# Kernel optimization log

Hardware: AMD Instinct MI355X
Metric: run time of the kernel (lower is better)

The kernel has to match this reference:

```python
import jax, jax.numpy as jnp
import numpy as np

B, L, H, V = 16, 512, 256, 32000
HALF = H // 2
EPS_LN = 1e-5
EPS_NORM = 1e-12


def setup_inputs() -> dict:
    key = jax.random.key(0)
    ks = jax.random.split(key, 9)
    s = 0.02
    return {
        "seq": jax.random.randint(ks[0], (B, L), 0, V),
        "embed": jax.random.normal(ks[1], (V, H), jnp.float32) * s,
        "W1": jax.random.normal(ks[2], (2 * H, H), jnp.float32) * s,
        "b1": jnp.zeros((2 * H,), jnp.float32),
        "W2": jax.random.normal(ks[3], (H, 2 * H), jnp.float32) * s,
        "b2": jnp.zeros((H,), jnp.float32),
        "gamma": jnp.ones((H,), jnp.float32),
        "beta": jnp.zeros((H,), jnp.float32),
        "W_sem": jax.random.normal(ks[4], (HALF, H), jnp.float32) * s,
        "W_epi": jax.random.normal(ks[5], (HALF, H), jnp.float32) * s,
        "W_rp": jax.random.normal(ks[6], (H, H), jnp.float32) * s,
        "b_rp": jnp.zeros((H,), jnp.float32),
        "W_out": jax.random.normal(ks[7], (V, H), jnp.float32) * s,
        "b_out": jnp.zeros((V,), jnp.float32),
    }


def _l2norm(x):
    # F.normalize(dim=-1): x / max(||x||, eps)
    n = jnp.sqrt(jnp.sum(x * x, axis=-1, keepdims=True))
    return x / jnp.maximum(n, EPS_NORM)


def reference(seq, embed, W1, b1, W2, b2, gamma, beta, W_sem, W_epi, W_rp, b_rp, W_out, b_out):
    h = embed[seq]                                   # [B, L, H]
    ff = jnp.maximum(h @ W1.T + b1, 0.0) @ W2.T + b2  # MLP with 2H hidden
    x = h + ff
    mu = jnp.mean(x, axis=-1, keepdims=True)
    var = jnp.var(x, axis=-1, keepdims=True)
    h = (x - mu) / jnp.sqrt(var + EPS_LN) * gamma + beta  # LayerNorm

    ks_all = jnp.einsum('blh,kh->blk', h, W_sem)     # [B, L, HALF]
    ke_all = jnp.einsum('blh,kh->blk', h, W_epi)

    def step(carry, kv):
        M_s, M_e = carry
        k_s, k_e = kv                                 # [B, HALF] each
        kns = _l2norm(k_s)
        kne = _l2norm(k_e)
        vps = jnp.einsum('bij,bj->bi', M_s, kns)      # read from fast weights
        vpe = jnp.einsum('bij,bj->bi', M_e, kne)
        M_s = M_s + jnp.einsum('bi,bj->bij', k_s - vps, kns)  # delta-rule write
        M_e = M_e + jnp.einsum('bi,bj->bij', k_e - vpe, kne)
        return (M_s, M_e), None

    M0 = jnp.zeros((B, HALF, HALF), h.dtype)
    # scan over timesteps 0..L-2 (time-major)
    (M_s, M_e), _ = jax.lax.scan(
        step, (M0, M0),
        (jnp.swapaxes(ks_all[:, :-1], 0, 1), jnp.swapaxes(ke_all[:, :-1], 0, 1)))

    cs = jnp.einsum('bij,bj->bi', M_s, ks_all[:, -1])  # read with last-token query
    ce = jnp.einsum('bij,bj->bi', M_e, ke_all[:, -1])
    c = jnp.concatenate([cs, ce], axis=-1)             # [B, H]
    r = c @ W_rp.T + b_rp
    return r @ W_out.T + b_out                          # [B, V]
```

## Files before the change

kernel.cpp:

```cpp
#include <hip/hip_runtime.h>

#define B_ 16
#define L_ 512
#define H_ 256
#define V_ 32000
#define HALF_ 128

typedef __attribute__((ext_vector_type(8))) short short8;
typedef __attribute__((ext_vector_type(4))) float floatx4;

__device__ __forceinline__ unsigned short f2bf(float x) {
  unsigned int u = __float_as_uint(x);
  unsigned int r = (u + 0x7FFFu + ((u >> 16) & 1u)) >> 16;
  return (unsigned short)r;
}

template <int CTRL>
__device__ __forceinline__ float dpp_xor_add(float x) {
  int y = __builtin_amdgcn_mov_dpp(__float_as_int(x), CTRL, 0xf, 0xf, true);
  return x + __int_as_float(y);
}

__device__ __forceinline__ float redu16(float p) {
  p = dpp_xor_add<0xB1>(p);
  p = dpp_xor_add<0x4E>(p);
  p = dpp_xor_add<0x141>(p);
  p = dpp_xor_add<0x140>(p);
  return p;
}

__device__ __forceinline__ void async_cp16(const float* g, float* l) {
  __builtin_amdgcn_global_load_lds(
      (const __attribute__((address_space(1))) void*)g,
      (__attribute__((address_space(3))) void*)l, 16, 0, 0);
}

__device__ __forceinline__ uint4 load8cvt(const float* p) {
  float4 a = ((const float4*)p)[0];
  float4 b = ((const float4*)p)[1];
  uint4 r;
  r.x = (unsigned)f2bf(a.x) | ((unsigned)f2bf(a.y) << 16);
  r.y = (unsigned)f2bf(a.z) | ((unsigned)f2bf(a.w) << 16);
  r.z = (unsigned)f2bf(b.x) | ((unsigned)f2bf(b.y) << 16);
  r.w = (unsigned)f2bf(b.z) | ((unsigned)f2bf(b.w) << 16);
  return r;
}

__global__ __launch_bounds__(256) void gemm1_kernel(const int* __restrict__ seq,
                                                    const float* __restrict__ embed,
                                                    const float* __restrict__ W1,
                                                    const float* __restrict__ b1,
                                                    unsigned short* __restrict__ a1b) {
  __shared__ unsigned short As[128 * 40];
  __shared__ unsigned short Bs[128 * 40];
  int tid = threadIdx.x;
  int wave = tid >> 6, lane = tid & 63;
  int wm = (wave >> 1) * 64, wn = (wave & 1) * 64;
  int quad = lane >> 4, l15 = lane & 15;
  int bm = blockIdx.y * 128, bn = blockIdx.x * 128;
  int sr = tid >> 2, sq = tid & 3;

  int tok0 = seq[bm + sr];
  int tok1 = seq[bm + 64 + sr];

  floatx4 zero = {0.f, 0.f, 0.f, 0.f};
  floatx4 acc[4][4];
#pragma unroll
  for (int fi = 0; fi < 4; fi++)
#pragma unroll
    for (int fj = 0; fj < 4; fj++) acc[fi][fj] = zero;

  uint4 av0 = load8cvt(embed + (size_t)tok0 * H_ + sq * 8);
  uint4 av1 = load8cvt(embed + (size_t)tok1 * H_ + sq * 8);
  uint4 bv0 = load8cvt(W1 + (size_t)(bn + sr) * 256 + sq * 8);
  uint4 bv1 = load8cvt(W1 + (size_t)(bn + 64 + sr) * 256 + sq * 8);

  for (int k0 = 0; k0 < 256; k0 += 32) {
    __syncthreads();
    *(uint4*)(As + sr * 40 + sq * 8) = av0;
    *(uint4*)(As + (64 + sr) * 40 + sq * 8) = av1;
    *(uint4*)(Bs + sr * 40 + sq * 8) = bv0;
    *(uint4*)(Bs + (64 + sr) * 40 + sq * 8) = bv1;
    __syncthreads();
    if (k0 + 32 < 256) {
      av0 = load8cvt(embed + (size_t)tok0 * H_ + k0 + 32 + sq * 8);
      av1 = load8cvt(embed + (size_t)tok1 * H_ + k0 + 32 + sq * 8);
      bv0 = load8cvt(W1 + (size_t)(bn + sr) * 256 + k0 + 32 + sq * 8);
      bv1 = load8cvt(W1 + (size_t)(bn + 64 + sr) * 256 + k0 + 32 + sq * 8);
    }
    short8 af[4], bf[4];
#pragma unroll
    for (int f = 0; f < 4; f++) {
      af[f] = *(const short8*)(As + (wm + f * 16 + l15) * 40 + quad * 8);
      bf[f] = *(const short8*)(Bs + (wn + f * 16 + l15) * 40 + quad * 8);
    }
#pragma unroll
    for (int fi = 0; fi < 4; fi++)
#pragma unroll
      for (int fj = 0; fj < 4; fj++)
        acc[fi][fj] = __builtin_amdgcn_mfma_f32_16x16x32_bf16(af[fi], bf[fj], acc[fi][fj], 0, 0, 0);
  }

#pragma unroll
  for (int fi = 0; fi < 4; fi++) {
#pragma unroll
    for (int fj = 0; fj < 4; fj++) {
      int col = bn + wn + fj * 16 + l15;
      float bb = b1[col];
#pragma unroll
      for (int rg = 0; rg < 4; rg++) {
        int row = bm + wm + fi * 16 + quad * 4 + rg;
        float v = fmaxf(acc[fi][fj][rg] + bb, 0.f);
        a1b[(size_t)row * 512 + col] = f2bf(v);
      }
    }
  }
}

__global__ __launch_bounds__(256) void mlp2_kernel(const unsigned short* __restrict__ a1b,
                                                   const float* __restrict__ W2,
                                                   const float* __restrict__ b2,
                                                   const int* __restrict__ seq,
                                                   const float* __restrict__ embed,
                                                   const float* __restrict__ gamma,
                                                   const float* __restrict__ beta,
                                                   unsigned short* __restrict__ hnb) {
  __shared__ unsigned short As[32 * 40];
  __shared__ unsigned short Bs[256 * 40];
  __shared__ float stats[2][2][32];
  int tid = threadIdx.x;
  int wave = tid >> 6, lane = tid & 63;
  int wm = (wave >> 1) * 16, wnh = wave & 1, wn = wnh * 128;
  int quad = lane >> 4, l15 = lane & 15;
  int bm = blockIdx.x * 32;
  int sr = tid >> 2, sq = tid & 3;

  floatx4 zero = {0.f, 0.f, 0.f, 0.f};
  floatx4 acc[8];
#pragma unroll
  for (int fj = 0; fj < 8; fj++) acc[fj] = zero;

  uint4 av, bv[4];
  if (tid < 128) av = *(const uint4*)(a1b + (size_t)(bm + sr) * 512 + sq * 8);
#pragma unroll
  for (int q = 0; q < 4; q++) {
    int unit = q * 256 + tid;
    bv[q] = load8cvt(W2 + (size_t)(unit >> 2) * 512 + (unit & 3) * 8);
  }

  for (int k0 = 0; k0 < 512; k0 += 32) {
    __syncthreads();
    if (tid < 128) *(uint4*)(As + sr * 40 + sq * 8) = av;
#pragma unroll
    for (int q = 0; q < 4; q++) {
      int unit = q * 256 + tid;
      *(uint4*)(Bs + (unit >> 2) * 40 + (unit & 3) * 8) = bv[q];
    }
    __syncthreads();
    if (k0 + 32 < 512) {
      if (tid < 128) av = *(const uint4*)(a1b + (size_t)(bm + sr) * 512 + k0 + 32 + sq * 8);
#pragma unroll
      for (int q = 0; q < 4; q++) {
        int unit = q * 256 + tid;
        bv[q] = load8cvt(W2 + (size_t)(unit >> 2) * 512 + k0 + 32 + (unit & 3) * 8);
      }
    }
    short8 af = *(const short8*)(As + (wm + l15) * 40 + quad * 8);
    short8 bf[8];
#pragma unroll
    for (int fj = 0; fj < 8; fj++)
      bf[fj] = *(const short8*)(Bs + (wn + fj * 16 + l15) * 40 + quad * 8);
#pragma unroll
    for (int fj = 0; fj < 8; fj++)
      acc[fj] = __builtin_amdgcn_mfma_f32_16x16x32_bf16(af, bf[fj], acc[fj], 0, 0, 0);
  }

  int seqv[4];
#pragma unroll
  for (int rg = 0; rg < 4; rg++) seqv[rg] = seq[bm + wm + quad * 4 + rg];
  float v[8][4];
#pragma unroll
  for (int fj = 0; fj < 8; fj++) {
    int col = wn + fj * 16 + l15;
    float bb = b2[col];
#pragma unroll
    for (int rg = 0; rg < 4; rg++)
      v[fj][rg] = acc[fj][rg] + bb + embed[(size_t)seqv[rg] * H_ + col];
  }
  float s_[4], q_[4];
#pragma unroll
  for (int rg = 0; rg < 4; rg++) {
    float s = 0.f, q = 0.f;
#pragma unroll
    for (int fj = 0; fj < 8; fj++) {
      s += v[fj][rg];
      q += v[fj][rg] * v[fj][rg];
    }
    s_[rg] = redu16(s);
    q_[rg] = redu16(q);
  }
  if (l15 == 0) {
#pragma unroll
    for (int rg = 0; rg < 4; rg++) {
      int rlocal = wm + quad * 4 + rg;
      stats[wnh][0][rlocal] = s_[rg];
      stats[wnh][1][rlocal] = q_[rg];
    }
  }
  __syncthreads();
  float mu[4], inv[4];
#pragma unroll
  for (int rg = 0; rg < 4; rg++) {
    int rlocal = wm + quad * 4 + rg;
    float sum = stats[0][0][rlocal] + stats[1][0][rlocal];
    float ssq = stats[0][1][rlocal] + stats[1][1][rlocal];
    mu[rg] = sum * (1.f / H_);
    float var = ssq * (1.f / H_) - mu[rg] * mu[rg];
    inv[rg] = rsqrtf(var + 1e-5f);
  }
#pragma unroll
  for (int fj = 0; fj < 8; fj++) {
    int col = wn + fj * 16 + l15;
    float g = gamma[col], be = beta[col];
#pragma unroll
    for (int rg = 0; rg < 4; rg++) {
      int row = bm + wm + quad * 4 + rg;
      float y = (v[fj][rg] - mu[rg]) * inv[rg] * g + be;
      hnb[(size_t)row * H_ + col] = f2bf(y);
    }
  }
}

__global__ __launch_bounds__(256) void kproj_kernel(const unsigned short* __restrict__ hnb,
                                                    const float* __restrict__ Ws,
                                                    const float* __restrict__ We,
                                                    float* __restrict__ khat,
                                                    float* __restrict__ kT) {
  __shared__ unsigned short As[32 * 40];
  __shared__ unsigned short Bs[256 * 40];
  int tid = threadIdx.x;
  int wave = tid >> 6, lane = tid & 63;
  int wm = (wave >> 1) * 16, wnh = wave & 1, wn = wnh * 128;
  int quad = lane >> 4, l15 = lane & 15;
  int bm = blockIdx.x * 32;
  int sr = tid >> 2, sq = tid & 3;

  floatx4 zero = {0.f, 0.f, 0.f, 0.f};
  floatx4 acc[8];
#pragma unroll
  for (int fj = 0; fj < 8; fj++) acc[fj] = zero;

  uint4 av, bv[4];
  if (tid < 128) av = *(const uint4*)(hnb + (size_t)(bm + sr) * H_ + sq * 8);
#pragma unroll
  for (int q = 0; q < 4; q++) {
    int unit = q * 256 + tid;
    int row = unit >> 2;
    const float* src = (row < 128) ? (Ws + (size_t)row * H_) : (We + (size_t)(row - 128) * H_);
    bv[q] = load8cvt(src + (unit & 3) * 8);
  }

  for (int k0 = 0; k0 < 256; k0 += 32) {
    __syncthreads();
    if (tid < 128) *(uint4*)(As + sr * 40 + sq * 8) = av;
#pragma unroll
    for (int q = 0; q < 4; q++) {
      int unit = q * 256 + tid;
      *(uint4*)(Bs + (unit >> 2) * 40 + (unit & 3) * 8) = bv[q];
    }
    __syncthreads();
    if (k0 + 32 < 256) {
      if (tid < 128) av = *(const uint4*)(hnb + (size_t)(bm + sr) * H_ + k0 + 32 + sq * 8);
#pragma unroll
      for (int q = 0; q < 4; q++) {
        int unit = q * 256 + tid;
        int row = unit >> 2;
        const float* src = (row < 128) ? (Ws + (size_t)row * H_) : (We + (size_t)(row - 128) * H_);
        bv[q] = load8cvt(src + k0 + 32 + (unit & 3) * 8);
      }
    }
    short8 af = *(const short8*)(As + (wm + l15) * 40 + quad * 8);
    short8 bf[8];
#pragma unroll
    for (int fj = 0; fj < 8; fj++)
      bf[fj] = *(const short8*)(Bs + (wn + fj * 16 + l15) * 40 + quad * 8);
#pragma unroll
    for (int fj = 0; fj < 8; fj++)
      acc[fj] = __builtin_amdgcn_mfma_f32_16x16x32_bf16(af, bf[fj], acc[fj], 0, 0, 0);
  }

  int b = bm >> 9;
  int idxm = b * 2 + wnh;
  int tloc0 = (bm & 511) + wm + quad * 4;
  float inv[4];
#pragma unroll
  for (int rg = 0; rg < 4; rg++) {
    float ssq = 0.f;
#pragma unroll
    for (int fj = 0; fj < 8; fj++) ssq += acc[fj][rg] * acc[fj][rg];
    ssq = redu16(ssq);
    inv[rg] = 1.f / fmaxf(sqrtf(ssq), 1e-12f);
  }
#pragma unroll
  for (int fj = 0; fj < 8; fj++) {
    int ch = fj * 16 + l15;
    int j = ch >> 2, e = ch & 3;
    int pj = (j & 1) ? (16 + (j >> 1)) : (j >> 1);
    int pcol = pj * 4 + e;
#pragma unroll
    for (int rg = 0; rg < 4; rg++)
      khat[((size_t)idxm * L_ + tloc0 + rg) * HALF_ + pcol] = acc[fj][rg] * inv[rg];
    float4 raw = {acc[fj][0], acc[fj][1], acc[fj][2], acc[fj][3]};
    *(float4*)(kT + (size_t)idxm * (HALF_ * L_) + (size_t)ch * L_ + tloc0) = raw;
  }
}

#define STEP(KP, KR)                                                     \
  do {                                                                   \
    float t0_ = m[0] * KP[0] + m[1] * KP[1];                             \
    float t1_ = m[2] * KP[2] + m[3] * KP[3];                             \
    float t2_ = m[4] * KP[4] + m[5] * KP[5];                             \
    float t3_ = m[6] * KP[6] + m[7] * KP[7];                             \
    float p_ = (t0_ + t1_) + (t2_ + t3_);                                \
    p_ = redu16(p_);                                                     \
    float s_ = (KR) - p_;                                                \
    m[0] += s_ * KP[0]; m[1] += s_ * KP[1]; m[2] += s_ * KP[2];          \
    m[3] += s_ * KP[3]; m[4] += s_ * KP[4]; m[5] += s_ * KP[5];          \
    m[6] += s_ * KP[6]; m[7] += s_ * KP[7];                              \
  } while (0)

__global__ __launch_bounds__(512) void scan_kernel(const float* __restrict__ khat,
                                                   const float* __restrict__ kT,
                                                   float* __restrict__ c) {
  __shared__ float sk[2][64 * 128];
  int bid = blockIdx.x;
  int idxm = bid & 31;
  int rgp = bid >> 5;
  int b = idxm >> 1, mat = idxm & 1;
  const float* kh = khat + (size_t)idxm * L_ * HALF_;
  const float* kTi = kT + (size_t)idxm * HALF_ * L_;

  int tid = threadIdx.x;
  int wave = tid >> 6, lane = tid & 63;
  int seg = tid & 15, rl = tid >> 4;
  int r = rgp * 32 + rl;
  int c0 = seg * 8;
  const float* krow = kTi + (size_t)r * L_;

  float m[8];
#pragma unroll
  for (int g = 0; g < 8; g++) m[g] = 0.f;

  {
#pragma unroll
    for (int j = 0; j < 4; j++) {
      int slice = j * 8 + wave;
      async_cp16(kh + slice * 256 + lane * 4, &sk[0][slice * 256] + lane * 4);
    }
  }
  __syncthreads();

  float4 krn = *(const float4*)(krow);
  const float* lb = &sk[0][0] + seg * 4;

  for (int ch = 0; ch < 7; ch++) {
    {
#pragma unroll
      for (int j = 0; j < 4; j++) {
        int slice = j * 8 + wave;
        async_cp16(kh + (size_t)(ch + 1) * 8192 + slice * 256 + lane * 4,
                   &sk[(ch + 1) & 1][slice * 256] + lane * 4);
      }
    }
    const float* base = lb + (ch & 1) * 8192;
    float pk[4][8];
#pragma unroll
    for (int u = 0; u < 4; u++) {
      *(float4*)&pk[u][0] = *(const float4*)(base + u * 128);
      *(float4*)&pk[u][4] = *(const float4*)(base + u * 128 + 64);
    }
    for (int g = 0; g < 15; g++) {
      float4 krc = krn;
      krn = *(const float4*)(krow + ch * 64 + g * 4 + 4);
#pragma unroll
      for (int u = 0; u < 4; u++) {
        STEP(pk[u], ((u == 0) ? krc.x : (u == 1) ? krc.y : (u == 2) ? krc.z : krc.w));
        int tn = g * 4 + u + 4;
        *(float4*)&pk[u][0] = *(const float4*)(base + tn * 128);
        *(float4*)&pk[u][4] = *(const float4*)(base + tn * 128 + 64);
      }
    }
    {
      float4 krc = krn;
      krn = *(const float4*)(krow + ch * 64 + 64);
      STEP(pk[0], krc.x);
      STEP(pk[1], krc.y);
      STEP(pk[2], krc.z);
      STEP(pk[3], krc.w);
    }
    __syncthreads();
  }

  {
    const float* base = lb + 8192;
    float pk[4][8];
#pragma unroll
    for (int u = 0; u < 4; u++) {
      *(float4*)&pk[u][0] = *(const float4*)(base + u * 128);
      *(float4*)&pk[u][4] = *(const float4*)(base + u * 128 + 64);
    }
    for (int g = 0; g < 15; g++) {
      float4 krc = krn;
      krn = *(const float4*)(krow + 448 + g * 4 + 4);
#pragma unroll
      for (int u = 0; u < 4; u++) {
        STEP(pk[u], ((u == 0) ? krc.x : (u == 1) ? krc.y : (u == 2) ? krc.z : krc.w));
        int tn = g * 4 + u + 4;
        *(float4*)&pk[u][0] = *(const float4*)(base + tn * 128);
        *(float4*)&pk[u][4] = *(const float4*)(base + tn * 128 + 64);
      }
    }
    float4 krc = krn;
    STEP(pk[0], krc.x);
    STEP(pk[1], krc.y);
    STEP(pk[2], krc.z);
  }

  float q[8];
#pragma unroll
  for (int j = 0; j < 8; j++) q[j] = kTi[(size_t)(c0 + j) * L_ + 511];
  float t0 = m[0] * q[0] + m[1] * q[1];
  float t1 = m[2] * q[2] + m[3] * q[3];
  float t2 = m[4] * q[4] + m[5] * q[5];
  float t3 = m[6] * q[6] + m[7] * q[7];
  float p = redu16((t0 + t1) + (t2 + t3));
  if (seg == 0) c[(size_t)b * H_ + mat * HALF_ + r] = p;
}

__global__ void rp_kernel(const float* __restrict__ c, const float* __restrict__ Wrp,
                          const float* __restrict__ brp, float* __restrict__ r) {
  int b = blockIdx.x;
  int n = threadIdx.x;
  __shared__ float cs[H_];
  cs[n] = c[(size_t)b * H_ + n];
  __syncthreads();
  const float4* w4 = (const float4*)(Wrp + (size_t)n * H_);
  const float4* c4 = (const float4*)cs;
  float acc = 0.f;
#pragma unroll 8
  for (int k = 0; k < H_ / 4; k++) {
    float4 w = w4[k], cc = c4[k];
    acc += w.x * cc.x + w.y * cc.y + w.z * cc.z + w.w * cc.w;
  }
  r[(size_t)b * H_ + n] = acc + brp[n];
}

__global__ __launch_bounds__(256) void out_kernel(const float* __restrict__ r,
                                                  const float* __restrict__ Wout,
                                                  const float* __restrict__ bout,
                                                  float* __restrict__ out) {
  __shared__ float rs[16 * 272];
  __shared__ float obuf[16 * 68];
  int tid = threadIdx.x;
#pragma unroll
  for (int q = 0; q < 16; q++) {
    int idx = q * 256 + tid;
    int bb = idx >> 8, cc = idx & 255;
    rs[bb * 272 + cc + 4 * (cc >> 6)] = r[idx];
  }
  __syncthreads();
  int row = tid >> 2, part = tid & 3;
  int v = blockIdx.x * 64 + row;
  const float4* w4 = (const float4*)(Wout + (size_t)v * H_ + part * 64);
  float acc[16];
#pragma unroll
  for (int bb = 0; bb < 16; bb++) acc[bb] = 0.f;
#pragma unroll 4
  for (int j = 0; j < 16; j++) {
    float4 w = w4[j];
#pragma unroll
    for (int bb = 0; bb < 16; bb++) {
      float4 rv = *(const float4*)&rs[bb * 272 + part * 68 + j * 4];
      acc[bb] += w.x * rv.x + w.y * rv.y + w.z * rv.z + w.w * rv.w;
    }
  }
  float bo = bout[v];
#pragma unroll
  for (int bb = 0; bb < 16; bb++) {
    acc[bb] = dpp_xor_add<0xB1>(acc[bb]);
    acc[bb] = dpp_xor_add<0x4E>(acc[bb]);
  }
#pragma unroll
  for (int q = 0; q < 4; q++) {
    int bb = part * 4 + q;
    obuf[bb * 68 + row] = acc[bb] + bo;
  }
  __syncthreads();
#pragma unroll
  for (int q = 0; q < 4; q++) {
    int idx = q * 256 + tid;
    int bb = idx >> 6, vl = idx & 63;
    out[(size_t)bb * V_ + blockIdx.x * 64 + vl] = obuf[bb * 68 + vl];
  }
}

extern "C" void kernel_launch(void* const* d_in, const int* in_sizes, int n_in,
                              void* d_out, int out_size, void* d_ws, size_t ws_size,
                              hipStream_t stream) {
  const int* seq = (const int*)d_in[0];
  const float* embed = (const float*)d_in[1];
  const float* W1 = (const float*)d_in[2];
  const float* b1 = (const float*)d_in[3];
  const float* W2 = (const float*)d_in[4];
  const float* b2 = (const float*)d_in[5];
  const float* gamma = (const float*)d_in[6];
  const float* beta = (const float*)d_in[7];
  const float* Wsem = (const float*)d_in[8];
  const float* Wepi = (const float*)d_in[9];
  const float* Wrp = (const float*)d_in[10];
  const float* brp = (const float*)d_in[11];
  const float* Wout = (const float*)d_in[12];
  const float* bout = (const float*)d_in[13];
  float* out = (float*)d_out;

  float* ws = (float*)d_ws;
  unsigned short* a1b = (unsigned short*)ws;
  unsigned short* hnb = (unsigned short*)(ws + 2097152);
  float* khat = ws + 3145728;
  float* kT = ws + 5242880;
  float* c = ws + 7340032;
  float* r = ws + 7344128;

  gemm1_kernel<<<dim3(4, 64), 256, 0, stream>>>(seq, embed, W1, b1, a1b);
  mlp2_kernel<<<256, 256, 0, stream>>>(a1b, W2, b2, seq, embed, gamma, beta, hnb);
  kproj_kernel<<<256, 256, 0, stream>>>(hnb, Wsem, Wepi, khat, kT);
  scan_kernel<<<128, 512, 0, stream>>>(khat, kT, c);
  rp_kernel<<<16, 256, 0, stream>>>(c, Wrp, brp, r);
  out_kernel<<<500, 256, 0, stream>>>(r, Wout, bout, out);
}
```

Before: 243.9 us.

## Chunk delta-rule scan with Gram-matrix triangular solve, fuse kproj into MLP

The sequential delta-rule scan is replaced by a chunked form. For each 16-token chunk, an MFMA computes the Gram matrix of the normalized keys, the corrections are found by forward substitution using readlane broadcasts, and the fast-weight updates are applied in a batch. This removes the per-step dependent read-update chain. The key-projection GEMM is fused into the MLP/LayerNorm kernel through an LDS-resident normalized tile, and a prep kernel pre-converts the weights to bf16 once per call. The scan grid also changes to 256 blocks of 256 threads. The Gram matrix is computed in bf16, which adds rounding error to the recurrence.

```diff
diff --git a/kernel.cpp b/kernel.cpp
--- a/kernel.cpp
+++ b/kernel.cpp
@@ -46,9 +46,23 @@
   return r;
 }
 
+__global__ __launch_bounds__(256) void prep_kernel(const float* __restrict__ W1,
+                                                   const float* __restrict__ W2,
+                                                   const float* __restrict__ Ws,
+                                                   const float* __restrict__ We,
+                                                   unsigned short* __restrict__ W1b,
+                                                   unsigned short* __restrict__ W2b,
+                                                   unsigned short* __restrict__ Wcb) {
+  int i = blockIdx.x * 256 + threadIdx.x;
+  if (i < 131072) W1b[i] = f2bf(W1[i]);
+  else if (i < 262144) W2b[i - 131072] = f2bf(W2[i - 131072]);
+  else if (i < 294912) Wcb[i - 262144] = f2bf(Ws[i - 262144]);
+  else Wcb[i - 262144] = f2bf(We[i - 294912]);
+}
+
 __global__ __launch_bounds__(256) void gemm1_kernel(const int* __restrict__ seq,
                                                     const float* __restrict__ embed,
-                                                    const float* __restrict__ W1,
+                                                    const unsigned short* __restrict__ W1b,
                                                     const float* __restrict__ b1,
                                                     unsigned short* __restrict__ a1b) {
   __shared__ unsigned short As[128 * 40];
@@ -72,8 +86,8 @@
 
   uint4 av0 = load8cvt(embed + (size_t)tok0 * H_ + sq * 8);
   uint4 av1 = load8cvt(embed + (size_t)tok1 * H_ + sq * 8);
-  uint4 bv0 = load8cvt(W1 + (size_t)(bn + sr) * 256 + sq * 8);
-  uint4 bv1 = load8cvt(W1 + (size_t)(bn + 64 + sr) * 256 + sq * 8);
+  uint4 bv0 = *(const uint4*)(W1b + (size_t)(bn + sr) * 256 + sq * 8);
+  uint4 bv1 = *(const uint4*)(W1b + (size_t)(bn + 64 + sr) * 256 + sq * 8);
 
   for (int k0 = 0; k0 < 256; k0 += 32) {
     __syncthreads();
@@ -85,8 +99,8 @@
     if (k0 + 32 < 256) {
       av0 = load8cvt(embed + (size_t)tok0 * H_ + k0 + 32 + sq * 8);
       av1 = load8cvt(embed + (size_t)tok1 * H_ + k0 + 32 + sq * 8);
-      bv0 = load8cvt(W1 + (size_t)(bn + sr) * 256 + k0 + 32 + sq * 8);
-      bv1 = load8cvt(W1 + (size_t)(bn + 64 + sr) * 256 + k0 + 32 + sq * 8);
+      bv0 = *(const uint4*)(W1b + (size_t)(bn + sr) * 256 + k0 + 32 + sq * 8);
+      bv1 = *(const uint4*)(W1b + (size_t)(bn + 64 + sr) * 256 + k0 + 32 + sq * 8);
     }
     short8 af[4], bf[4];
 #pragma unroll
@@ -117,16 +131,19 @@
   }
 }
 
-__global__ __launch_bounds__(256) void mlp2_kernel(const unsigned short* __restrict__ a1b,
-                                                   const float* __restrict__ W2,
+__global__ __launch_bounds__(256) void mlpk_kernel(const unsigned short* __restrict__ a1b,
+                                                   const unsigned short* __restrict__ W2b,
                                                    const float* __restrict__ b2,
                                                    const int* __restrict__ seq,
                                                    const float* __restrict__ embed,
                                                    const float* __restrict__ gamma,
                                                    const float* __restrict__ beta,
-                                                   unsigned short* __restrict__ hnb) {
+                                                   const unsigned short* __restrict__ Wcb,
+                                                   float* __restrict__ khat,
+                                                   float* __restrict__ kT) {
   __shared__ unsigned short As[32 * 40];
   __shared__ unsigned short Bs[256 * 40];
+  __shared__ unsigned short hnS[32 * 264];
   __shared__ float stats[2][2][32];
   int tid = threadIdx.x;
   int wave = tid >> 6, lane = tid & 63;
@@ -145,9 +162,8 @@
 #pragma unroll
   for (int q = 0; q < 4; q++) {
     int unit = q * 256 + tid;
-    bv[q] = load8cvt(W2 + (size_t)(unit >> 2) * 512 + (unit & 3) * 8);
-  }
-
+    bv[q] = *(const uint4*)(W2b + (size_t)(unit >> 2) * 512 + (unit & 3) * 8);
+  }
   for (int k0 = 0; k0 < 512; k0 += 32) {
     __syncthreads();
     if (tid < 128) *(uint4*)(As + sr * 40 + sq * 8) = av;
@@ -162,7 +178,7 @@
 #pragma unroll
       for (int q = 0; q < 4; q++) {
         int unit = q * 256 + tid;
-        bv[q] = load8cvt(W2 + (size_t)(unit >> 2) * 512 + k0 + 32 + (unit & 3) * 8);
+        bv[q] = *(const uint4*)(W2b + (size_t)(unit >> 2) * 512 + k0 + 32 + (unit & 3) * 8);
       }
     }
     short8 af = *(const short8*)(As + (wm + l15) * 40 + quad * 8);
@@ -208,61 +224,33 @@
     }
   }
   __syncthreads();
-  float mu[4], inv[4];
 #pragma unroll
   for (int rg = 0; rg < 4; rg++) {
     int rlocal = wm + quad * 4 + rg;
     float sum = stats[0][0][rlocal] + stats[1][0][rlocal];
     float ssq = stats[0][1][rlocal] + stats[1][1][rlocal];
-    mu[rg] = sum * (1.f / H_);
-    float var = ssq * (1.f / H_) - mu[rg] * mu[rg];
-    inv[rg] = rsqrtf(var + 1e-5f);
-  }
-#pragma unroll
-  for (int fj = 0; fj < 8; fj++) {
-    int col = wn + fj * 16 + l15;
-    float g = gamma[col], be = beta[col];
-#pragma unroll
-    for (int rg = 0; rg < 4; rg++) {
-      int row = bm + wm + quad * 4 + rg;
-      float y = (v[fj][rg] - mu[rg]) * inv[rg] * g + be;
-      hnb[(size_t)row * H_ + col] = f2bf(y);
-    }
-  }
-}
-
-__global__ __launch_bounds__(256) void kproj_kernel(const unsigned short* __restrict__ hnb,
-                                                    const float* __restrict__ Ws,
-                                                    const float* __restrict__ We,
-                                                    float* __restrict__ khat,
-                                                    float* __restrict__ kT) {
-  __shared__ unsigned short As[32 * 40];
-  __shared__ unsigned short Bs[256 * 40];
-  int tid = threadIdx.x;
-  int wave = tid >> 6, lane = tid & 63;
-  int wm = (wave >> 1) * 16, wnh = wave & 1, wn = wnh * 128;
-  int quad = lane >> 4, l15 = lane & 15;
-  int bm = blockIdx.x * 32;
-  int sr = tid >> 2, sq = tid & 3;
-
-  floatx4 zero = {0.f, 0.f, 0.f, 0.f};
-  floatx4 acc[8];
-#pragma unroll
-  for (int fj = 0; fj < 8; fj++) acc[fj] = zero;
-
-  uint4 av, bv[4];
-  if (tid < 128) av = *(const uint4*)(hnb + (size_t)(bm + sr) * H_ + sq * 8);
+    float mu = sum * (1.f / H_);
+    float var = ssq * (1.f / H_) - mu * mu;
+    float inv = rsqrtf(var + 1e-5f);
+#pragma unroll
+    for (int fj = 0; fj < 8; fj++) {
+      int col = wn + fj * 16 + l15;
+      float y = (v[fj][rg] - mu) * inv * gamma[col] + beta[col];
+      hnS[rlocal * 264 + col] = f2bf(y);
+    }
+  }
+  __syncthreads();
+
+  floatx4 acc2[8];
+#pragma unroll
+  for (int fj = 0; fj < 8; fj++) acc2[fj] = zero;
 #pragma unroll
   for (int q = 0; q < 4; q++) {
     int unit = q * 256 + tid;
-    int row = unit >> 2;
-    const float* src = (row < 128) ? (Ws + (size_t)row * H_) : (We + (size_t)(row - 128) * H_);
-    bv[q] = load8cvt(src + (unit & 3) * 8);
-  }
-
+    bv[q] = *(const uint4*)(Wcb + (size_t)(unit >> 2) * 256 + (unit & 3) * 8);
+  }
   for (int k0 = 0; k0 < 256; k0 += 32) {
     __syncthreads();
-    if (tid < 128) *(uint4*)(As + sr * 40 + sq * 8) = av;
 #pragma unroll
     for (int q = 0; q < 4; q++) {
       int unit = q * 256 + tid;
@@ -270,23 +258,20 @@
     }
     __syncthreads();
     if (k0 + 32 < 256) {
-      if (tid < 128) av = *(const uint4*)(hnb + (size_t)(bm + sr) * H_ + k0 + 32 + sq * 8);
 #pragma unroll
       for (int q = 0; q < 4; q++) {
         int unit = q * 256 + tid;
-        int row = unit >> 2;
-        const float* src = (row < 128) ? (Ws + (size_t)row * H_) : (We + (size_t)(row - 128) * H_);
-        bv[q] = load8cvt(src + k0 + 32 + (unit & 3) * 8);
+        bv[q] = *(const uint4*)(Wcb + (size_t)(unit >> 2) * 256 + k0 + 32 + (unit & 3) * 8);
       }
     }
-    short8 af = *(const short8*)(As + (wm + l15) * 40 + quad * 8);
+    short8 af = *(const short8*)(hnS + (wm + l15) * 264 + k0 + quad * 8);
     short8 bf[8];
 #pragma unroll
     for (int fj = 0; fj < 8; fj++)
       bf[fj] = *(const short8*)(Bs + (wn + fj * 16 + l15) * 40 + quad * 8);
 #pragma unroll
     for (int fj = 0; fj < 8; fj++)
-      acc[fj] = __builtin_amdgcn_mfma_f32_16x16x32_bf16(af, bf[fj], acc[fj], 0, 0, 0);
+      acc2[fj] = __builtin_amdgcn_mfma_f32_16x16x32_bf16(af, bf[fj], acc2[fj], 0, 0, 0);
   }
 
   int b = bm >> 9;
@@ -297,7 +282,7 @@
   for (int rg = 0; rg < 4; rg++) {
     float ssq = 0.f;
 #pragma unroll
-    for (int fj = 0; fj < 8; fj++) ssq += acc[fj][rg] * acc[fj][rg];
+    for (int fj = 0; fj < 8; fj++) ssq += acc2[fj][rg] * acc2[fj][rg];
     ssq = redu16(ssq);
     inv[rg] = 1.f / fmaxf(sqrtf(ssq), 1e-12f);
   }
@@ -309,33 +294,19 @@
     int pcol = pj * 4 + e;
 #pragma unroll
     for (int rg = 0; rg < 4; rg++)
-      khat[((size_t)idxm * L_ + tloc0 + rg) * HALF_ + pcol] = acc[fj][rg] * inv[rg];
-    float4 raw = {acc[fj][0], acc[fj][1], acc[fj][2], acc[fj][3]};
+      khat[((size_t)idxm * L_ + tloc0 + rg) * HALF_ + pcol] = acc2[fj][rg] * inv[rg];
+    float4 raw = {acc2[fj][0], acc2[fj][1], acc2[fj][2], acc2[fj][3]};
     *(float4*)(kT + (size_t)idxm * (HALF_ * L_) + (size_t)ch * L_ + tloc0) = raw;
   }
 }
 
-#define STEP(KP, KR)                                                     \
-  do {                                                                   \
-    float t0_ = m[0] * KP[0] + m[1] * KP[1];                             \
-    float t1_ = m[2] * KP[2] + m[3] * KP[3];                             \
-    float t2_ = m[4] * KP[4] + m[5] * KP[5];                             \
-    float t3_ = m[6] * KP[6] + m[7] * KP[7];                             \
-    float p_ = (t0_ + t1_) + (t2_ + t3_);                                \
-    p_ = redu16(p_);                                                     \
-    float s_ = (KR) - p_;                                                \
-    m[0] += s_ * KP[0]; m[1] += s_ * KP[1]; m[2] += s_ * KP[2];          \
-    m[3] += s_ * KP[3]; m[4] += s_ * KP[4]; m[5] += s_ * KP[5];          \
-    m[6] += s_ * KP[6]; m[7] += s_ * KP[7];                              \
-  } while (0)
-
-__global__ __launch_bounds__(512) void scan_kernel(const float* __restrict__ khat,
+__global__ __launch_bounds__(256) void scan_kernel(const float* __restrict__ khat,
                                                    const float* __restrict__ kT,
                                                    float* __restrict__ c) {
   __shared__ float sk[2][64 * 128];
   int bid = blockIdx.x;
   int idxm = bid & 31;
-  int rgp = bid >> 5;
+  int rg = bid >> 5;
   int b = idxm >> 1, mat = idxm & 1;
   const float* kh = khat + (size_t)idxm * L_ * HALF_;
   const float* kTi = kT + (size_t)idxm * HALF_ * L_;
@@ -343,7 +314,8 @@
   int tid = threadIdx.x;
   int wave = tid >> 6, lane = tid & 63;
   int seg = tid & 15, rl = tid >> 4;
-  int r = rgp * 32 + rl;
+  int l15 = lane & 15, quad = lane >> 4;
+  int r = rg * 16 + rl;
   int c0 = seg * 8;
   const float* krow = kTi + (size_t)r * L_;
 
@@ -351,80 +323,87 @@
 #pragma unroll
   for (int g = 0; g < 8; g++) m[g] = 0.f;
 
-  {
-#pragma unroll
-    for (int j = 0; j < 4; j++) {
-      int slice = j * 8 + wave;
-      async_cp16(kh + slice * 256 + lane * 4, &sk[0][slice * 256] + lane * 4);
-    }
-  }
+#pragma unroll
+  for (int j = 0; j < 8; j++)
+    async_cp16(kh + wave * 2048 + j * 256 + lane * 4, &sk[0][wave * 2048 + j * 256] + lane * 4);
+
+  float kr[16], nkr[16];
+#pragma unroll
+  for (int q = 0; q < 4; q++) *(float4*)&kr[q * 4] = *(const float4*)(krow + q * 4);
+
   __syncthreads();
 
-  float4 krn = *(const float4*)(krow);
   const float* lb = &sk[0][0] + seg * 4;
 
-  for (int ch = 0; ch < 7; ch++) {
-    {
-#pragma unroll
-      for (int j = 0; j < 4; j++) {
-        int slice = j * 8 + wave;
-        async_cp16(kh + (size_t)(ch + 1) * 8192 + slice * 256 + lane * 4,
-                   &sk[(ch + 1) & 1][slice * 256] + lane * 4);
+  auto do_chunk = [&](const float* bt, int gch, bool last) {
+    const float* gsrc = kh + (size_t)(gch * 16 + l15) * HALF_;
+    floatx4 g4 = {0.f, 0.f, 0.f, 0.f};
+#pragma unroll
+    for (int kc = 0; kc < 4; kc++) {
+      float4 x0 = *(const float4*)(gsrc + kc * 32 + quad * 8);
+      float4 x1 = *(const float4*)(gsrc + kc * 32 + quad * 8 + 4);
+      uint4 pkk;
+      pkk.x = (unsigned)f2bf(x0.x) | ((unsigned)f2bf(x0.y) << 16);
+      pkk.y = (unsigned)f2bf(x0.z) | ((unsigned)f2bf(x0.w) << 16);
+      pkk.z = (unsigned)f2bf(x1.x) | ((unsigned)f2bf(x1.y) << 16);
+      pkk.w = (unsigned)f2bf(x1.z) | ((unsigned)f2bf(x1.w) << 16);
+      short8 kf = *(short8*)&pkk;
+      g4 = __builtin_amdgcn_mfma_f32_16x16x32_bf16(kf, kf, g4, 0, 0, 0);
+    }
+    if (gch < 31) {
+#pragma unroll
+      for (int q = 0; q < 4; q++)
+        *(float4*)&nkr[q * 4] = *(const float4*)(krow + (gch + 1) * 16 + q * 4);
+    }
+    float pp[16];
+#pragma unroll
+    for (int i = 0; i < 16; i++) {
+      float4 ka = *(const float4*)(bt + i * 128);
+      float4 kb = *(const float4*)(bt + i * 128 + 64);
+      float t0 = m[0] * ka.x + m[1] * ka.y;
+      float t1 = m[2] * ka.z + m[3] * ka.w;
+      float t2 = m[4] * kb.x + m[5] * kb.y;
+      float t3 = m[6] * kb.z + m[7] * kb.w;
+      pp[i] = redu16((t0 + t1) + (t2 + t3));
+    }
+    float dd[16];
+#pragma unroll
+    for (int i = 0; i < 16; i++) dd[i] = kr[i] - pp[i];
+#pragma unroll
+    for (int j = 0; j < 15; j++) {
+#pragma unroll
+      for (int i = j + 1; i < 16; i++) {
+        int gv = __builtin_amdgcn_readlane(__float_as_int(g4[j & 3]), (j >> 2) * 16 + i);
+        dd[i] -= __int_as_float(gv) * dd[j];
       }
     }
-    const float* base = lb + (ch & 1) * 8192;
-    float pk[4][8];
-#pragma unroll
-    for (int u = 0; u < 4; u++) {
-      *(float4*)&pk[u][0] = *(const float4*)(base + u * 128);
-      *(float4*)&pk[u][4] = *(const float4*)(base + u * 128 + 64);
-    }
-    for (int g = 0; g < 15; g++) {
-      float4 krc = krn;
-      krn = *(const float4*)(krow + ch * 64 + g * 4 + 4);
-#pragma unroll
-      for (int u = 0; u < 4; u++) {
-        STEP(pk[u], ((u == 0) ? krc.x : (u == 1) ? krc.y : (u == 2) ? krc.z : krc.w));
-        int tn = g * 4 + u + 4;
-        *(float4*)&pk[u][0] = *(const float4*)(base + tn * 128);
-        *(float4*)&pk[u][4] = *(const float4*)(base + tn * 128 + 64);
-      }
-    }
-    {
-      float4 krc = krn;
-      krn = *(const float4*)(krow + ch * 64 + 64);
-      STEP(pk[0], krc.x);
-      STEP(pk[1], krc.y);
-      STEP(pk[2], krc.z);
-      STEP(pk[3], krc.w);
-    }
-    __syncthreads();
-  }
-
-  {
-    const float* base = lb + 8192;
-    float pk[4][8];
-#pragma unroll
-    for (int u = 0; u < 4; u++) {
-      *(float4*)&pk[u][0] = *(const float4*)(base + u * 128);
-      *(float4*)&pk[u][4] = *(const float4*)(base + u * 128 + 64);
-    }
-    for (int g = 0; g < 15; g++) {
-      float4 krc = krn;
-      krn = *(const float4*)(krow + 448 + g * 4 + 4);
-#pragma unroll
-      for (int u = 0; u < 4; u++) {
-        STEP(pk[u], ((u == 0) ? krc.x : (u == 1) ? krc.y : (u == 2) ? krc.z : krc.w));
-        int tn = g * 4 + u + 4;
-        *(float4*)&pk[u][0] = *(const float4*)(base + tn * 128);
-        *(float4*)&pk[u][4] = *(const float4*)(base + tn * 128 + 64);
-      }
-    }
-    float4 krc = krn;
-    STEP(pk[0], krc.x);
-    STEP(pk[1], krc.y);
-    STEP(pk[2], krc.z);
-  }
+#pragma unroll
+    for (int i = 0; i < 16; i++) {
+      if (last && i == 15) break;
+      float4 ka = *(const float4*)(bt + i * 128);
+      float4 kb = *(const float4*)(bt + i * 128 + 64);
+      m[0] += dd[i] * ka.x; m[1] += dd[i] * ka.y;
+      m[2] += dd[i] * ka.z; m[3] += dd[i] * ka.w;
+      m[4] += dd[i] * kb.x; m[5] += dd[i] * kb.y;
+      m[6] += dd[i] * kb.z; m[7] += dd[i] * kb.w;
+    }
+#pragma unroll
+    for (int q = 0; q < 16; q++) kr[q] = nkr[q];
+  };
+
+  for (int buf = 0; buf < 8; buf++) {
+    if (buf < 7) {
+#pragma unroll
+      for (int j = 0; j < 8; j++)
+        async_cp16(kh + (size_t)(buf + 1) * 8192 + wave * 2048 + j * 256 + lane * 4,
+                   &sk[(buf + 1) & 1][wave * 2048 + j * 256] + lane * 4);
+    }
+    const float* bb = lb + (buf & 1) * 8192;
+    int nsub = (buf == 7) ? 3 : 4;
+    for (int sub = 0; sub < nsub; sub++) do_chunk(bb + sub * 16 * 128, buf * 4 + sub, false);
+    __syncthreads();
+  }
+  do_chunk(lb + 8192 + 3 * 16 * 128, 31, true);
 
   float q[8];
 #pragma unroll
@@ -525,16 +504,18 @@
 
   float* ws = (float*)d_ws;
   unsigned short* a1b = (unsigned short*)ws;
-  unsigned short* hnb = (unsigned short*)(ws + 2097152);
-  float* khat = ws + 3145728;
-  float* kT = ws + 5242880;
-  float* c = ws + 7340032;
-  float* r = ws + 7344128;
-
-  gemm1_kernel<<<dim3(4, 64), 256, 0, stream>>>(seq, embed, W1, b1, a1b);
-  mlp2_kernel<<<256, 256, 0, stream>>>(a1b, W2, b2, seq, embed, gamma, beta, hnb);
-  kproj_kernel<<<256, 256, 0, stream>>>(hnb, Wsem, Wepi, khat, kT);
-  scan_kernel<<<128, 512, 0, stream>>>(khat, kT, c);
+  float* khat = ws + 2097152;
+  float* kT = ws + 4194304;
+  unsigned short* W1b = (unsigned short*)(ws + 6291456);
+  unsigned short* W2b = (unsigned short*)(ws + 6356992);
+  unsigned short* Wcb = (unsigned short*)(ws + 6422528);
+  float* c = ws + 6455296;
+  float* r = ws + 6459392;
+
+  prep_kernel<<<1280, 256, 0, stream>>>(W1, W2, Wsem, Wepi, W1b, W2b, Wcb);
+  gemm1_kernel<<<dim3(4, 64), 256, 0, stream>>>(seq, embed, W1b, b1, a1b);
+  mlpk_kernel<<<256, 256, 0, stream>>>(a1b, W2b, b2, seq, embed, gamma, beta, Wcb, khat, kT);
+  scan_kernel<<<256, 256, 0, stream>>>(khat, kT, c);
   rp_kernel<<<16, 256, 0, stream>>>(c, Wrp, brp, r);
   out_kernel<<<500, 256, 0, stream>>>(r, Wout, bout, out);
 }
```

Measured after the change: 305.3 us. 25.2% more time.
